# Kernel optimization log

Measured on AMD Instinct MI355X. Metric: run time of the kernel, lower is better.

## Reference

```python
import jax, jax.numpy as jnp
import numpy as np

N = 50000   # nodes
E = 600000  # edges
D = 128     # in_feats
H = 128     # n_hidden
C = 47      # n_classes


def setup_inputs() -> dict:
    key = jax.random.key(0)
    ks = jax.random.split(key, 12)
    x = jax.random.normal(ks[0], (N, D), dtype=jnp.float32)
    src = jax.random.randint(ks[1], (E,), 0, N, dtype=jnp.int32)
    dst = jax.random.randint(ks[2], (E,), 0, N, dtype=jnp.int32)
    def lin(k, fi, fo):
        s = 1.0 / np.sqrt(fi)
        return jax.random.uniform(k, (fi, fo), jnp.float32, -s, s)
    return {
        "x": x, "src": src, "dst": dst,
        "W_self0": lin(ks[3], D, H), "W_neigh0": lin(ks[4], D, H), "b0": jnp.zeros((H,), jnp.float32),
        "W_self1": lin(ks[5], H, H), "W_neigh1": lin(ks[6], H, H), "b1": jnp.zeros((H,), jnp.float32),
        "W_self2": lin(ks[7], H, C), "W_neigh2": lin(ks[8], H, C), "b2": jnp.zeros((C,), jnp.float32),
    }


def _sage_layer(h, src, dst, W_self, W_neigh, b, act):
    # gather neighbor (src) features, mean-aggregate onto dst nodes
    msum = jax.ops.segment_sum(h[src], dst, num_segments=N)           # [N, F]
    deg = jax.ops.segment_sum(jnp.ones((src.shape[0], 1), h.dtype), dst, num_segments=N)
    h_neigh = msum / jnp.maximum(deg, 1.0)                            # zero-degree -> 0
    out = h @ W_self + h_neigh @ W_neigh + b
    return jax.nn.relu(out) if act else out


def reference(x, src, dst, W_self0, W_neigh0, b0, W_self1, W_neigh1, b1, W_self2, W_neigh2, b2):
    h = _sage_layer(x, src, dst, W_self0, W_neigh0, b0, True)
    h = _sage_layer(h, src, dst, W_self1, W_neigh1, b1, True)
    h = _sage_layer(h, src, dst, W_self2, W_neigh2, b2, False)
    return h
```

## Files before the change

kernel.cpp:

```cpp
#include <hip/hip_runtime.h>
#include <hip/hip_bf16.h>


#define THREADS 256

typedef unsigned short u16;
typedef __attribute__((ext_vector_type(8))) short bf16x8;
typedef __attribute__((ext_vector_type(4))) float f32x4;

__device__ inline u16 f2bf(float f) {
    union { float f; unsigned u; } v; v.f = f;
    unsigned r = (v.u + 0x7FFFu + ((v.u >> 16) & 1u)) >> 16;
    return (u16)r;
}
__device__ inline float bf2f(u16 b) {
    union { unsigned u; float f; } v; v.u = ((unsigned)b) << 16;
    return v.f;
}
__device__ inline unsigned pack2(float a, float b) {
    return (unsigned)f2bf(a) | ((unsigned)f2bf(b) << 16);
}

#define GLDS16(gp, lp)                                                         \
    __builtin_amdgcn_global_load_lds(                                          \
        (const __attribute__((address_space(1))) void*)(gp),                   \
        (__attribute__((address_space(3))) void*)(lp), 16, 0, 0)

__global__ void k_count(const int* __restrict__ dst, int* __restrict__ deg, int E) {
    int e = blockIdx.x * blockDim.x + threadIdx.x;
    if (e < E) atomicAdd(&deg[dst[e]], 1);
}

__global__ void k_scan_block(const int* __restrict__ deg, int* __restrict__ off,
                             int* __restrict__ bsum, int n) {
    __shared__ int s[256];
    int t = threadIdx.x;
    int base = blockIdx.x * 1024 + t * 4;
    int v[4];
#pragma unroll
    for (int i = 0; i < 4; i++) v[i] = (base + i < n) ? deg[base + i] : 0;
    int sum = v[0] + v[1] + v[2] + v[3];
    int val = sum;
    s[t] = val;
    __syncthreads();
    for (int o = 1; o < 256; o <<= 1) {
        int x = (t >= o) ? s[t - o] : 0;
        __syncthreads();
        val += x;
        s[t] = val;
        __syncthreads();
    }
    int run = val - sum;
#pragma unroll
    for (int i = 0; i < 4; i++) {
        if (base + i < n) off[base + i] = run;
        run += v[i];
    }
    if (t == 255) bsum[blockIdx.x] = val;
}

__global__ void k_scan_bsum(int* __restrict__ bsum, int nb) {
    int lane = threadIdx.x;
    int carry = 0;
    for (int start = 0; start < nb; start += 64) {
        int i = start + lane;
        int orig = (i < nb) ? bsum[i] : 0;
        int v = orig;
#pragma unroll
        for (int o = 1; o < 64; o <<= 1) {
            int u = __shfl_up(v, o, 64);
            if (lane >= o) v += u;
        }
        if (i < nb) bsum[i] = carry + v - orig;
        carry += __shfl(v, 63, 64);
    }
}

__global__ void k_scan_add(int* __restrict__ off, const int* __restrict__ bsum, int n) {
    int t = threadIdx.x;
    int base = blockIdx.x * 1024 + t * 4;
    int add = bsum[blockIdx.x];
#pragma unroll
    for (int i = 0; i < 4; i++)
        if (base + i < n) off[base + i] += add;
}

__global__ void k_fill(const int* __restrict__ src, const int* __restrict__ dst,
                       const int* __restrict__ off, int* __restrict__ cur,
                       int* __restrict__ eidx, int E) {
    int e = blockIdx.x * blockDim.x + threadIdx.x;
    if (e < E) {
        int d = dst[e];
        int p = atomicAdd(&cur[d], 1);
        eidx[off[d] + p] = src[e];
    }
}

__global__ void k_prepX(const float* __restrict__ x, u16* __restrict__ hi,
                        u16* __restrict__ lo, int n32) {
    int i = blockIdx.x * blockDim.x + threadIdx.x;
    if (i >= n32) return;
    float4 v = ((const float4*)x)[i];
    float h0 = bf2f(f2bf(v.x)), h1 = bf2f(f2bf(v.y)), h2 = bf2f(f2bf(v.z)), h3 = bf2f(f2bf(v.w));
    uint2 hp, lp;
    hp.x = pack2(h0, h1); hp.y = pack2(h2, h3);
    lp.x = pack2(v.x - h0, v.y - h1); lp.y = pack2(v.z - h2, v.w - h3);
    ((uint2*)hi)[i] = hp;
    ((uint2*)lo)[i] = lp;
}

__global__ void k_prepW3(const float* __restrict__ Ws0, const float* __restrict__ Wn0,
                         const float* __restrict__ Ws1, const float* __restrict__ Wn1,
                         const float* __restrict__ Ws2, const float* __restrict__ Wn2,
                         u16* __restrict__ Bt) {
    int idx = blockIdx.x * blockDim.x + threadIdx.x;
    if (idx >= 3 * 128 * 256) return;
    int layer = idx >> 15;
    int within = idx & 32767;
    int col = within >> 8;
    int k = within & 255;
    const float* Ws = (layer == 0) ? Ws0 : (layer == 1) ? Ws1 : Ws2;
    const float* Wn = (layer == 0) ? Wn0 : (layer == 1) ? Wn1 : Wn2;
    int fout = (layer == 2) ? 47 : 128;
    float v = 0.f;
    if (col < fout) v = (k < 128) ? Ws[k * fout + col] : Wn[(k - 128) * fout + col];
    u16 h = f2bf(v);
    Bt[layer * 65536 + within] = h;
    Bt[layer * 65536 + 32768 + within] = f2bf(v - bf2f(h));
}

__global__ void k_aggregate(const u16* __restrict__ hi_in, const int* __restrict__ eidx,
                            const int* __restrict__ off, const int* __restrict__ deg,
                            u16* __restrict__ mhi, u16* __restrict__ mlo, int n) {
    int wv = blockIdx.x * 4 + (threadIdx.x >> 6);
    int lane = threadIdx.x & 63;
    int quarter = lane >> 4;
    int ql = lane & 15;
    int node = wv * 4 + quarter;
    if (node >= n) return;
    int cnt = deg[node];
    int base = off[node];
    const uint4* h4 = (const uint4*)hi_in;
    float acc[8];
#pragma unroll
    for (int i = 0; i < 8; i++) acc[i] = 0.f;
    for (int j = 0; j < cnt; j += 8) {
        int s[8];
        float m[8];
#pragma unroll
        for (int u = 0; u < 8; u++) {
            int jj = j + u;
            s[u] = eidx[base + (jj < cnt ? jj : 0)];
            m[u] = (jj < cnt) ? 1.f : 0.f;
        }
        uint4 v[8];
#pragma unroll
        for (int u = 0; u < 8; u++) v[u] = h4[(size_t)s[u] * 16 + ql];
#pragma unroll
        for (int u = 0; u < 8; u++) {
            acc[0] = fmaf(m[u], bf2f((u16)(v[u].x & 0xffffu)), acc[0]);
            acc[1] = fmaf(m[u], bf2f((u16)(v[u].x >> 16)), acc[1]);
            acc[2] = fmaf(m[u], bf2f((u16)(v[u].y & 0xffffu)), acc[2]);
            acc[3] = fmaf(m[u], bf2f((u16)(v[u].y >> 16)), acc[3]);
            acc[4] = fmaf(m[u], bf2f((u16)(v[u].z & 0xffffu)), acc[4]);
            acc[5] = fmaf(m[u], bf2f((u16)(v[u].z >> 16)), acc[5]);
            acc[6] = fmaf(m[u], bf2f((u16)(v[u].w & 0xffffu)), acc[6]);
            acc[7] = fmaf(m[u], bf2f((u16)(v[u].w >> 16)), acc[7]);
        }
    }
    float iv = 1.0f / (float)(cnt > 1 ? cnt : 1);
    float a[8], r[8];
#pragma unroll
    for (int i = 0; i < 8; i++) {
        a[i] = acc[i] * iv;
        r[i] = bf2f(f2bf(a[i]));
    }
    uint4 hp, lp;
    hp.x = pack2(a[0], a[1]); hp.y = pack2(a[2], a[3]);
    hp.z = pack2(a[4], a[5]); hp.w = pack2(a[6], a[7]);
    lp.x = pack2(a[0] - r[0], a[1] - r[1]); lp.y = pack2(a[2] - r[2], a[3] - r[3]);
    lp.z = pack2(a[4] - r[4], a[5] - r[5]); lp.w = pack2(a[6] - r[6], a[7] - r[7]);
    ((uint4*)mhi)[(size_t)node * 16 + ql] = hp;
    ((uint4*)mlo)[(size_t)node * 16 + ql] = lp;
}

__global__ __launch_bounds__(256) void k_gemm_mfma(
    const u16* __restrict__ Ahi_s, const u16* __restrict__ Alo_s,
    const u16* __restrict__ Ahi_n, const u16* __restrict__ Alo_n,
    const u16* __restrict__ Bthi, const u16* __restrict__ Btlo,
    const float* __restrict__ bias, float* __restrict__ out_f32,
    u16* __restrict__ out_hi, u16* __restrict__ out_lo, int n, int fout, int relu) {
    __shared__ u16 sAhi[64 * 32];
    __shared__ u16 sAlo[64 * 32];
    __shared__ u16 sBhi[128 * 32];
    __shared__ u16 sBlo[128 * 32];

    int t = threadIdx.x;
    int w = t >> 6;
    int lane = t & 63;
    int wr = w >> 1, wc = w & 1;
    size_t row0 = (size_t)blockIdx.x * 64;

    f32x4 acc[2][4];
#pragma unroll
    for (int r = 0; r < 2; r++)
#pragma unroll
        for (int c = 0; c < 4; c++) acc[r][c] = (f32x4){0.f, 0.f, 0.f, 0.f};

    for (int kk = 0; kk < 256; kk += 32) {
        const u16* Phi = (kk < 128) ? Ahi_s : Ahi_n;
        const u16* Plo = (kk < 128) ? Alo_s : Alo_n;
        int kc = kk & 127;
        __syncthreads();
        {
            int r = w * 16 + (lane >> 2);
            int cb = (lane & 3) * 8;
            GLDS16(Phi + (row0 + r) * 128 + kc + cb, &sAhi[r * 32 + cb]);
            GLDS16(Plo + (row0 + r) * 128 + kc + cb, &sAlo[r * 32 + cb]);
        }
#pragma unroll
        for (int i = 0; i < 2; i++) {
            int c = w * 32 + i * 16 + (lane >> 2);
            int cb = (lane & 3) * 8;
            GLDS16(Bthi + (size_t)c * 256 + kk + cb, &sBhi[c * 32 + cb]);
            GLDS16(Btlo + (size_t)c * 256 + kk + cb, &sBlo[c * 32 + cb]);
        }
        __syncthreads();

        bf16x8 a_hi[2], a_lo[2], b_hi[4], b_lo[4];
        int q8 = (lane >> 4) * 8;
#pragma unroll
        for (int r = 0; r < 2; r++) {
            int ad = (wr * 32 + r * 16 + (lane & 15)) * 32 + q8;
            a_hi[r] = *(const bf16x8*)&sAhi[ad];
            a_lo[r] = *(const bf16x8*)&sAlo[ad];
        }
#pragma unroll
        for (int c = 0; c < 4; c++) {
            int ad = (wc * 64 + c * 16 + (lane & 15)) * 32 + q8;
            b_hi[c] = *(const bf16x8*)&sBhi[ad];
            b_lo[c] = *(const bf16x8*)&sBlo[ad];
        }
#pragma unroll
        for (int r = 0; r < 2; r++)
#pragma unroll
            for (int c = 0; c < 4; c++) {
                acc[r][c] = __builtin_amdgcn_mfma_f32_16x16x32_bf16(
                    a_hi[r], b_hi[c], acc[r][c], 0, 0, 0);
                acc[r][c] = __builtin_amdgcn_mfma_f32_16x16x32_bf16(
                    a_hi[r], b_lo[c], acc[r][c], 0, 0, 0);
                acc[r][c] = __builtin_amdgcn_mfma_f32_16x16x32_bf16(
                    a_lo[r], b_hi[c], acc[r][c], 0, 0, 0);
            }
    }

    int quad = lane >> 4;
    int lcol = lane & 15;
#pragma unroll
    for (int r = 0; r < 2; r++) {
#pragma unroll
        for (int c = 0; c < 4; c++) {
            int col = wc * 64 + c * 16 + lcol;
            float bv = (col < fout) ? bias[col] : 0.f;
#pragma unroll
            for (int g = 0; g < 4; g++) {
                size_t row = row0 + wr * 32 + r * 16 + quad * 4 + g;
                if (row >= (size_t)n || col >= fout) continue;
                float v = acc[r][c][g] + bv;
                if (relu) v = v > 0.f ? v : 0.f;
                if (out_f32) out_f32[row * fout + col] = v;
                if (out_hi) {
                    u16 h = f2bf(v);
                    out_hi[row * 128 + col] = h;
                    out_lo[row * 128 + col] = f2bf(v - bf2f(h));
                }
            }
        }
    }
}

extern "C" void kernel_launch(void* const* d_in, const int* in_sizes, int n_in,
                              void* d_out, int out_size, void* d_ws, size_t ws_size,
                              hipStream_t stream) {
    const float* x = (const float*)d_in[0];
    const int* src = (const int*)d_in[1];
    const int* dst = (const int*)d_in[2];
    const float* Ws0 = (const float*)d_in[3];
    const float* Wn0 = (const float*)d_in[4];
    const float* b0 = (const float*)d_in[5];
    const float* Ws1 = (const float*)d_in[6];
    const float* Wn1 = (const float*)d_in[7];
    const float* b1 = (const float*)d_in[8];
    const float* Ws2 = (const float*)d_in[9];
    const float* Wn2 = (const float*)d_in[10];
    const float* b2 = (const float*)d_in[11];
    float* out = (float*)d_out;

    const int N = in_sizes[0] / 128;
    const int E = in_sizes[1];
    const int Npad = ((N + 63) / 64) * 64;

    char* p = (char*)d_ws;
    u16* P0hi = (u16*)p; p += (size_t)Npad * 128 * 2;
    u16* P0lo = (u16*)p; p += (size_t)Npad * 128 * 2;
    u16* P1hi = (u16*)p; p += (size_t)Npad * 128 * 2;
    u16* P1lo = (u16*)p; p += (size_t)Npad * 128 * 2;
    u16* Mhi = (u16*)p; p += (size_t)Npad * 128 * 2;
    u16* Mlo = (u16*)p; p += (size_t)Npad * 128 * 2;
    u16* Bt = (u16*)p; p += 3 * 2 * 128 * 256 * 2;
    int* deg = (int*)p; p += (size_t)N * 4;
    int* cur = (int*)p; p += (size_t)N * 4;
    int* off = (int*)p; p += (size_t)N * 4;
    int* eidx = (int*)p; p += (size_t)E * 4;
    int* bsum = (int*)p;

    const int nbE = (E + THREADS - 1) / THREADS;
    const int nbScan = (N + 1023) / 1024;
    const int nbAgg = (N + 15) / 16;
    const int nbGemm = (N + 63) / 64;
    const int nbPX = (N * 32 + THREADS - 1) / THREADS;
    const int nbPW = (3 * 128 * 256 + THREADS - 1) / THREADS;

    hipMemsetAsync(deg, 0, (size_t)2 * N * sizeof(int), stream);

    k_count<<<nbE, THREADS, 0, stream>>>(dst, deg, E);
    k_scan_block<<<nbScan, 256, 0, stream>>>(deg, off, bsum, N);
    k_scan_bsum<<<1, 64, 0, stream>>>(bsum, nbScan);
    k_scan_add<<<nbScan, 256, 0, stream>>>(off, bsum, N);
    k_fill<<<nbE, THREADS, 0, stream>>>(src, dst, off, cur, eidx, E);

    k_prepX<<<nbPX, THREADS, 0, stream>>>(x, P0hi, P0lo, N * 32);
    k_prepW3<<<nbPW, THREADS, 0, stream>>>(Ws0, Wn0, Ws1, Wn1, Ws2, Wn2, Bt);

    k_aggregate<<<nbAgg, 256, 0, stream>>>(P0hi, eidx, off, deg, Mhi, Mlo, N);
    k_gemm_mfma<<<nbGemm, 256, 0, stream>>>(P0hi, P0lo, Mhi, Mlo,
                                            Bt + 0 * 65536, Bt + 0 * 65536 + 32768, b0,
                                            (float*)nullptr, P1hi, P1lo, N, 128, 1);
    k_aggregate<<<nbAgg, 256, 0, stream>>>(P1hi, eidx, off, deg, Mhi, Mlo, N);
    k_gemm_mfma<<<nbGemm, 256, 0, stream>>>(P1hi, P1lo, Mhi, Mlo,
                                            Bt + 1 * 65536, Bt + 1 * 65536 + 32768, b1,
                                            (float*)nullptr, P0hi, P0lo, N, 128, 1);
    k_aggregate<<<nbAgg, 256, 0, stream>>>(P0hi, eidx, off, deg, Mhi, Mlo, N);
    k_gemm_mfma<<<nbGemm, 256, 0, stream>>>(P0hi, P0lo, Mhi, Mlo,
                                            Bt + 2 * 65536, Bt + 2 * 65536 + 32768, b2,
                                            out, (u16*)nullptr, (u16*)nullptr, N, 47, 0);
}
```

Measured before the change: 309.3 us.

## Fuse neighbor mean-aggregation into the SAGE GEMM kernel via shared memory

Merges the separate aggregation kernel into the MFMA GEMM kernel. Each 64-row block first computes the self-feature half of the product, then gathers and averages neighbor features for its rows, writes the hi/lo bf16 split into XOR-swizzled shared memory, and runs the neighbor half of the K loop from LDS. This drops the global round trip of the aggregated M buffers and three kernel launches per forward pass. In exchange, LDS use grows to 48 KB per block, which can lower occupancy, and the irregular gather now runs inside the GEMM blocks with less parallelism per block.

New measurement: 325.4 us. 1.05x slower.

```diff
diff --git a/kernel.cpp b/kernel.cpp
--- a/kernel.cpp
+++ b/kernel.cpp
@@ -129,71 +129,14 @@
     Bt[layer * 65536 + 32768 + within] = f2bf(v - bf2f(h));
 }
 
-__global__ void k_aggregate(const u16* __restrict__ hi_in, const int* __restrict__ eidx,
-                            const int* __restrict__ off, const int* __restrict__ deg,
-                            u16* __restrict__ mhi, u16* __restrict__ mlo, int n) {
-    int wv = blockIdx.x * 4 + (threadIdx.x >> 6);
-    int lane = threadIdx.x & 63;
-    int quarter = lane >> 4;
-    int ql = lane & 15;
-    int node = wv * 4 + quarter;
-    if (node >= n) return;
-    int cnt = deg[node];
-    int base = off[node];
-    const uint4* h4 = (const uint4*)hi_in;
-    float acc[8];
-#pragma unroll
-    for (int i = 0; i < 8; i++) acc[i] = 0.f;
-    for (int j = 0; j < cnt; j += 8) {
-        int s[8];
-        float m[8];
-#pragma unroll
-        for (int u = 0; u < 8; u++) {
-            int jj = j + u;
-            s[u] = eidx[base + (jj < cnt ? jj : 0)];
-            m[u] = (jj < cnt) ? 1.f : 0.f;
-        }
-        uint4 v[8];
-#pragma unroll
-        for (int u = 0; u < 8; u++) v[u] = h4[(size_t)s[u] * 16 + ql];
-#pragma unroll
-        for (int u = 0; u < 8; u++) {
-            acc[0] = fmaf(m[u], bf2f((u16)(v[u].x & 0xffffu)), acc[0]);
-            acc[1] = fmaf(m[u], bf2f((u16)(v[u].x >> 16)), acc[1]);
-            acc[2] = fmaf(m[u], bf2f((u16)(v[u].y & 0xffffu)), acc[2]);
-            acc[3] = fmaf(m[u], bf2f((u16)(v[u].y >> 16)), acc[3]);
-            acc[4] = fmaf(m[u], bf2f((u16)(v[u].z & 0xffffu)), acc[4]);
-            acc[5] = fmaf(m[u], bf2f((u16)(v[u].z >> 16)), acc[5]);
-            acc[6] = fmaf(m[u], bf2f((u16)(v[u].w & 0xffffu)), acc[6]);
-            acc[7] = fmaf(m[u], bf2f((u16)(v[u].w >> 16)), acc[7]);
-        }
-    }
-    float iv = 1.0f / (float)(cnt > 1 ? cnt : 1);
-    float a[8], r[8];
-#pragma unroll
-    for (int i = 0; i < 8; i++) {
-        a[i] = acc[i] * iv;
-        r[i] = bf2f(f2bf(a[i]));
-    }
-    uint4 hp, lp;
-    hp.x = pack2(a[0], a[1]); hp.y = pack2(a[2], a[3]);
-    hp.z = pack2(a[4], a[5]); hp.w = pack2(a[6], a[7]);
-    lp.x = pack2(a[0] - r[0], a[1] - r[1]); lp.y = pack2(a[2] - r[2], a[3] - r[3]);
-    lp.z = pack2(a[4] - r[4], a[5] - r[5]); lp.w = pack2(a[6] - r[6], a[7] - r[7]);
-    ((uint4*)mhi)[(size_t)node * 16 + ql] = hp;
-    ((uint4*)mlo)[(size_t)node * 16 + ql] = lp;
-}
-
-__global__ __launch_bounds__(256) void k_gemm_mfma(
+__global__ __launch_bounds__(256) void k_sage_fused(
     const u16* __restrict__ Ahi_s, const u16* __restrict__ Alo_s,
-    const u16* __restrict__ Ahi_n, const u16* __restrict__ Alo_n,
+    const int* __restrict__ eidx, const int* __restrict__ off,
+    const int* __restrict__ deg,
     const u16* __restrict__ Bthi, const u16* __restrict__ Btlo,
     const float* __restrict__ bias, float* __restrict__ out_f32,
     u16* __restrict__ out_hi, u16* __restrict__ out_lo, int n, int fout, int relu) {
-    __shared__ u16 sAhi[64 * 32];
-    __shared__ u16 sAlo[64 * 32];
-    __shared__ u16 sBhi[128 * 32];
-    __shared__ u16 sBlo[128 * 32];
+    __shared__ u16 smem[24576];
 
     int t = threadIdx.x;
     int w = t >> 6;
@@ -207,39 +150,133 @@
 #pragma unroll
         for (int c = 0; c < 4; c++) acc[r][c] = (f32x4){0.f, 0.f, 0.f, 0.f};
 
-    for (int kk = 0; kk < 256; kk += 32) {
-        const u16* Phi = (kk < 128) ? Ahi_s : Ahi_n;
-        const u16* Plo = (kk < 128) ? Alo_s : Alo_n;
-        int kc = kk & 127;
+    int q8 = (lane >> 4) * 8;
+
+    for (int kk = 0; kk < 128; kk += 32) {
         __syncthreads();
         {
             int r = w * 16 + (lane >> 2);
             int cb = (lane & 3) * 8;
-            GLDS16(Phi + (row0 + r) * 128 + kc + cb, &sAhi[r * 32 + cb]);
-            GLDS16(Plo + (row0 + r) * 128 + kc + cb, &sAlo[r * 32 + cb]);
+            GLDS16(Ahi_s + (row0 + r) * 128 + kk + cb, &smem[r * 32 + cb]);
+            GLDS16(Alo_s + (row0 + r) * 128 + kk + cb, &smem[2048 + r * 32 + cb]);
         }
 #pragma unroll
         for (int i = 0; i < 2; i++) {
             int c = w * 32 + i * 16 + (lane >> 2);
             int cb = (lane & 3) * 8;
-            GLDS16(Bthi + (size_t)c * 256 + kk + cb, &sBhi[c * 32 + cb]);
-            GLDS16(Btlo + (size_t)c * 256 + kk + cb, &sBlo[c * 32 + cb]);
+            GLDS16(Bthi + (size_t)c * 256 + kk + cb, &smem[16384 + c * 32 + cb]);
+            GLDS16(Btlo + (size_t)c * 256 + kk + cb, &smem[20480 + c * 32 + cb]);
         }
         __syncthreads();
 
         bf16x8 a_hi[2], a_lo[2], b_hi[4], b_lo[4];
-        int q8 = (lane >> 4) * 8;
 #pragma unroll
         for (int r = 0; r < 2; r++) {
             int ad = (wr * 32 + r * 16 + (lane & 15)) * 32 + q8;
-            a_hi[r] = *(const bf16x8*)&sAhi[ad];
-            a_lo[r] = *(const bf16x8*)&sAlo[ad];
+            a_hi[r] = *(const bf16x8*)&smem[ad];
+            a_lo[r] = *(const bf16x8*)&smem[2048 + ad];
         }
 #pragma unroll
         for (int c = 0; c < 4; c++) {
             int ad = (wc * 64 + c * 16 + (lane & 15)) * 32 + q8;
-            b_hi[c] = *(const bf16x8*)&sBhi[ad];
-            b_lo[c] = *(const bf16x8*)&sBlo[ad];
+            b_hi[c] = *(const bf16x8*)&smem[16384 + ad];
+            b_lo[c] = *(const bf16x8*)&smem[20480 + ad];
+        }
+#pragma unroll
+        for (int r = 0; r < 2; r++)
+#pragma unroll
+            for (int c = 0; c < 4; c++) {
+                acc[r][c] = __builtin_amdgcn_mfma_f32_16x16x32_bf16(
+                    a_hi[r], b_hi[c], acc[r][c], 0, 0, 0);
+                acc[r][c] = __builtin_amdgcn_mfma_f32_16x16x32_bf16(
+                    a_hi[r], b_lo[c], acc[r][c], 0, 0, 0);
+                acc[r][c] = __builtin_amdgcn_mfma_f32_16x16x32_bf16(
+                    a_lo[r], b_hi[c], acc[r][c], 0, 0, 0);
+            }
+    }
+
+    __syncthreads();
+    {
+        int quarter = lane >> 4;
+        int ql = lane & 15;
+        const uint4* h4 = (const uint4*)Ahi_s;
+#pragma unroll 1
+        for (int i = 0; i < 4; i++) {
+            int rloc = w * 16 + i * 4 + quarter;
+            int node = (int)row0 + rloc;
+            int cnt = 0, base = 0;
+            if (node < n) { cnt = deg[node]; base = off[node]; }
+            float accf[8];
+#pragma unroll
+            for (int z = 0; z < 8; z++) accf[z] = 0.f;
+            for (int j = 0; j < cnt; j += 8) {
+                int s[8];
+                float m[8];
+#pragma unroll
+                for (int u = 0; u < 8; u++) {
+                    int jj = j + u;
+                    s[u] = eidx[base + (jj < cnt ? jj : 0)];
+                    m[u] = (jj < cnt) ? 1.f : 0.f;
+                }
+                uint4 v[8];
+#pragma unroll
+                for (int u = 0; u < 8; u++) v[u] = h4[(size_t)s[u] * 16 + ql];
+#pragma unroll
+                for (int u = 0; u < 8; u++) {
+                    accf[0] = fmaf(m[u], bf2f((u16)(v[u].x & 0xffffu)), accf[0]);
+                    accf[1] = fmaf(m[u], bf2f((u16)(v[u].x >> 16)), accf[1]);
+                    accf[2] = fmaf(m[u], bf2f((u16)(v[u].y & 0xffffu)), accf[2]);
+                    accf[3] = fmaf(m[u], bf2f((u16)(v[u].y >> 16)), accf[3]);
+                    accf[4] = fmaf(m[u], bf2f((u16)(v[u].z & 0xffffu)), accf[4]);
+                    accf[5] = fmaf(m[u], bf2f((u16)(v[u].z >> 16)), accf[5]);
+                    accf[6] = fmaf(m[u], bf2f((u16)(v[u].w & 0xffffu)), accf[6]);
+                    accf[7] = fmaf(m[u], bf2f((u16)(v[u].w >> 16)), accf[7]);
+                }
+            }
+            float iv = 1.0f / (float)(cnt > 1 ? cnt : 1);
+            float a[8], rr[8];
+#pragma unroll
+            for (int z = 0; z < 8; z++) {
+                a[z] = accf[z] * iv;
+                rr[z] = bf2f(f2bf(a[z]));
+            }
+            uint4 hp, lp;
+            hp.x = pack2(a[0], a[1]); hp.y = pack2(a[2], a[3]);
+            hp.z = pack2(a[4], a[5]); hp.w = pack2(a[6], a[7]);
+            lp.x = pack2(a[0] - rr[0], a[1] - rr[1]); lp.y = pack2(a[2] - rr[2], a[3] - rr[3]);
+            lp.z = pack2(a[4] - rr[4], a[5] - rr[5]); lp.w = pack2(a[6] - rr[6], a[7] - rr[7]);
+            int sw = ql ^ (rloc & 7);
+            *(uint4*)&smem[rloc * 128 + sw * 8] = hp;
+            *(uint4*)&smem[8192 + rloc * 128 + sw * 8] = lp;
+        }
+    }
+    __syncthreads();
+
+    for (int kk = 128; kk < 256; kk += 32) {
+        __syncthreads();
+#pragma unroll
+        for (int i = 0; i < 2; i++) {
+            int c = w * 32 + i * 16 + (lane >> 2);
+            int cb = (lane & 3) * 8;
+            GLDS16(Bthi + (size_t)c * 256 + kk + cb, &smem[16384 + c * 32 + cb]);
+            GLDS16(Btlo + (size_t)c * 256 + kk + cb, &smem[20480 + c * 32 + cb]);
+        }
+        __syncthreads();
+
+        bf16x8 a_hi[2], a_lo[2], b_hi[4], b_lo[4];
+        int kslot = (kk - 128) >> 3;
+#pragma unroll
+        for (int r = 0; r < 2; r++) {
+            int row = wr * 32 + r * 16 + (lane & 15);
+            int ad = row * 128 + (((kslot + (lane >> 4)) ^ (row & 7)) << 3);
+            a_hi[r] = *(const bf16x8*)&smem[ad];
+            a_lo[r] = *(const bf16x8*)&smem[8192 + ad];
+        }
+#pragma unroll
+        for (int c = 0; c < 4; c++) {
+            int ad = (wc * 64 + c * 16 + (lane & 15)) * 32 + q8;
+            b_hi[c] = *(const bf16x8*)&smem[16384 + ad];
+            b_lo[c] = *(const bf16x8*)&smem[20480 + ad];
         }
 #pragma unroll
         for (int r = 0; r < 2; r++)
@@ -305,8 +342,6 @@
     u16* P0lo = (u16*)p; p += (size_t)Npad * 128 * 2;
     u16* P1hi = (u16*)p; p += (size_t)Npad * 128 * 2;
     u16* P1lo = (u16*)p; p += (size_t)Npad * 128 * 2;
-    u16* Mhi = (u16*)p; p += (size_t)Npad * 128 * 2;
-    u16* Mlo = (u16*)p; p += (size_t)Npad * 128 * 2;
     u16* Bt = (u16*)p; p += 3 * 2 * 128 * 256 * 2;
     int* deg = (int*)p; p += (size_t)N * 4;
     int* cur = (int*)p; p += (size_t)N * 4;
@@ -316,7 +351,6 @@
 
     const int nbE = (E + THREADS - 1) / THREADS;
     const int nbScan = (N + 1023) / 1024;
-    const int nbAgg = (N + 15) / 16;
     const int nbGemm = (N + 63) / 64;
     const int nbPX = (N * 32 + THREADS - 1) / THREADS;
     const int nbPW = (3 * 128 * 256 + THREADS - 1) / THREADS;
@@ -332,16 +366,13 @@
     k_prepX<<<nbPX, THREADS, 0, stream>>>(x, P0hi, P0lo, N * 32);
     k_prepW3<<<nbPW, THREADS, 0, stream>>>(Ws0, Wn0, Ws1, Wn1, Ws2, Wn2, Bt);
 
-    k_aggregate<<<nbAgg, 256, 0, stream>>>(P0hi, eidx, off, deg, Mhi, Mlo, N);
-    k_gemm_mfma<<<nbGemm, 256, 0, stream>>>(P0hi, P0lo, Mhi, Mlo,
-                                            Bt + 0 * 65536, Bt + 0 * 65536 + 32768, b0,
-                                            (float*)nullptr, P1hi, P1lo, N, 128, 1);
-    k_aggregate<<<nbAgg, 256, 0, stream>>>(P1hi, eidx, off, deg, Mhi, Mlo, N);
-    k_gemm_mfma<<<nbGemm, 256, 0, stream>>>(P1hi, P1lo, Mhi, Mlo,
-                                            Bt + 1 * 65536, Bt + 1 * 65536 + 32768, b1,
-                                            (float*)nullptr, P0hi, P0lo, N, 128, 1);
-    k_aggregate<<<nbAgg, 256, 0, stream>>>(P0hi, eidx, off, deg, Mhi, Mlo, N);
-    k_gemm_mfma<<<nbGemm, 256, 0, stream>>>(P0hi, P0lo, Mhi, Mlo,
-                                            Bt + 2 * 65536, Bt + 2 * 65536 + 32768, b2,
-                                            out, (u16*)nullptr, (u16*)nullptr, N, 47, 0);
-}
+    k_sage_fused<<<nbGemm, 256, 0, stream>>>(P0hi, P0lo, eidx, off, deg,
+                                             Bt + 0 * 65536, Bt + 0 * 65536 + 32768, b0,
+                                             (float*)nullptr, P1hi, P1lo, N, 128, 1);
+    k_sage_fused<<<nbGemm, 256, 0, stream>>>(P1hi, P1lo, eidx, off, deg,
+                                             Bt + 1 * 65536, Bt + 1 * 65536 + 32768, b1,
+                                             (float*)nullptr, P0hi, P0lo, N, 128, 1);
+    k_sage_fused<<<nbGemm, 256, 0, stream>>>(P0hi, P0lo, eidx, off, deg,
+                                             Bt + 2 * 65536, Bt + 2 * 65536 + 32768, b2,
+                                             out, (u16*)nullptr, (u16*)nullptr, N, 47, 0);
+}
```
